# Optimization experiments

Measured on AMD Instinct MI355X. Metric: run time of the kernel, lower is better.

The kernel has to match this reference:

```python
import jax, jax.numpy as jnp
import numpy as np

N_NODES = 100000
N_EDGES = 3200000
N_FEAT = 300
HIDDEN = 32
N_CLASSES = 10


def setup_inputs() -> dict:
    key = jax.random.key(0)
    k1, k2, k3, k4 = jax.random.split(key, 4)
    x = jax.random.normal(k1, (N_NODES, N_FEAT), dtype=jnp.float32)
    edge_index = jax.random.randint(k2, (2, N_EDGES), 0, N_NODES, dtype=jnp.int64)
    # Glorot-ish init for weights
    W1 = jax.random.normal(k3, (N_FEAT, HIDDEN), dtype=jnp.float32) * (1.0 / np.sqrt(N_FEAT))
    b1 = jnp.zeros((HIDDEN,), dtype=jnp.float32)
    W2 = jax.random.normal(k4, (HIDDEN, N_CLASSES), dtype=jnp.float32) * (1.0 / np.sqrt(HIDDEN))
    b2 = jnp.zeros((N_CLASSES,), dtype=jnp.float32)
    return {"x": x, "edge_index": edge_index, "W1": W1, "b1": b1, "W2": W2, "b2": b2}


def reference(x, edge_index, W1, b1, W2, b2):
    N = x.shape[0]
    # GCNConv default: add self-loops, symmetric normalization deg^-1/2 A deg^-1/2
    loops = jnp.arange(N, dtype=edge_index.dtype)
    src = jnp.concatenate([edge_index[0], loops])  # message sources
    dst = jnp.concatenate([edge_index[1], loops])  # aggregation targets

    deg = jax.ops.segment_sum(jnp.ones(dst.shape, dtype=x.dtype), dst, num_segments=N)
    dinv = jnp.where(deg > 0, jax.lax.rsqrt(deg), 0.0)
    norm = dinv[src] * dinv[dst]  # [E+N]

    def gcn_conv(h, W, b):
        h = h @ W                                   # [N, out] dense GEMM first (linear-then-propagate)
        msg = h[src] * norm[:, None]                # gather + scale
        out = jax.ops.segment_sum(msg, dst, num_segments=N)  # scatter-add aggregate
        return out + b

    h = jnp.tanh(gcn_conv(x, W1, b1))
    # dropout p=0.5 is identity in eval mode (training=False)
    logits = gcn_conv(h, W2, b2)
    return jax.nn.log_softmax(logits, axis=1)
```

## Files before the change

kernel.cpp:

```cpp
#include <hip/hip_runtime.h>
#include <math.h>
#include <float.h>

#define NFEAT 300
#define HID 32
#define NCLS 10
#define GP 16
#define BSZ 128
#define TILE 8192
#define XS 264

typedef unsigned int uint;

__device__ __forceinline__ unsigned short f2bf(float f) {
    uint u = __float_as_uint(f);
    u += 0x7FFFu + ((u >> 16) & 1u);
    return (unsigned short)(u >> 16);
}
__device__ __forceinline__ uint pack2(float a, float b) {
    return (uint)f2bf(a) | ((uint)f2bf(b) << 16);
}
__device__ __forceinline__ float4 cvt4(uint2 v) {
    return make_float4(__uint_as_float(v.x << 16),
                       __uint_as_float(v.x & 0xFFFF0000u),
                       __uint_as_float(v.y << 16),
                       __uint_as_float(v.y & 0xFFFF0000u));
}

__global__ void k_zero_i(int* __restrict__ p, int n) {
    int i = blockIdx.x * 256 + threadIdx.x;
    if (i < n) p[i] = 0;
}

__global__ __launch_bounds__(256) void k_bhist(const int* __restrict__ ei, int E, int NB,
                                               int* __restrict__ bcnt) {
    __shared__ int h[1024];
    for (int i = threadIdx.x; i < NB; i += 256) h[i] = 0;
    __syncthreads();
    for (long long i = (long long)blockIdx.x * 256 + threadIdx.x; i < E;
         i += (long long)gridDim.x * 256)
        atomicAdd(&h[ei[E + i] >> 7], 1);
    __syncthreads();
    for (int i = threadIdx.x; i < NB; i += 256) {
        int v = h[i];
        if (v) atomicAdd(&bcnt[i], v);
    }
}

__global__ void k_bscan(const int* __restrict__ bcnt, int NB, int E,
                        int* __restrict__ bases, int* __restrict__ bcur) {
    __shared__ int s[1024];
    int tid = threadIdx.x;
    int v = (tid < NB) ? bcnt[tid] : 0;
    s[tid] = v;
    __syncthreads();
    for (int off = 1; off < 1024; off <<= 1) {
        int t = (tid >= off) ? s[tid - off] : 0;
        __syncthreads();
        s[tid] += t;
        __syncthreads();
    }
    if (tid < NB) {
        int ex = s[tid] - v;
        bases[tid] = ex;
        bcur[tid] = ex;
        if (tid == NB - 1) bases[NB] = E;
    }
}

__global__ __launch_bounds__(256) void k_part(const int* __restrict__ ei, int E, int NB,
                                              int* __restrict__ bcur, int* __restrict__ pp) {
    __shared__ int hist[1024], lbase[1024], gbase[1024], lcur[1024];
    __shared__ int stage[TILE], tgt[TILE];
    int* part = gbase;
    int tid = threadIdx.x;
    long long t0 = (long long)blockIdx.x * TILE;
    int nE = (int)(((long long)E - t0 < TILE) ? ((long long)E - t0) : TILE);

    for (int b = tid; b < NB; b += 256) hist[b] = 0;
    __syncthreads();
    for (int i = tid; i < nE; i += 256) {
        int d = ei[E + t0 + i];
        atomicAdd(&hist[d >> 7], 1);
    }
    __syncthreads();
    int i0 = tid * 4;
    int c0 = (i0 + 0 < NB) ? hist[i0 + 0] : 0;
    int c1 = (i0 + 1 < NB) ? hist[i0 + 1] : 0;
    int c2 = (i0 + 2 < NB) ? hist[i0 + 2] : 0;
    int c3 = (i0 + 3 < NB) ? hist[i0 + 3] : 0;
    int sum = c0 + c1 + c2 + c3;
    part[tid] = sum;
    __syncthreads();
    for (int off = 1; off < 256; off <<= 1) {
        int t = (tid >= off) ? part[tid - off] : 0;
        __syncthreads();
        part[tid] += t;
        __syncthreads();
    }
    int ex = part[tid] - sum;
    if (i0 + 0 < NB) { lbase[i0 + 0] = ex; ex += c0; }
    if (i0 + 1 < NB) { lbase[i0 + 1] = ex; ex += c1; }
    if (i0 + 2 < NB) { lbase[i0 + 2] = ex; ex += c2; }
    if (i0 + 3 < NB) { lbase[i0 + 3] = ex; ex += c3; }
    __syncthreads();
    for (int b = tid; b < NB; b += 256) {
        int h = hist[b];
        gbase[b] = h ? atomicAdd(&bcur[b], h) : 0;
        lcur[b] = 0;
    }
    __syncthreads();
    for (int i = tid; i < nE; i += 256) {
        int s = ei[t0 + i];
        int d = ei[E + t0 + i];
        int b = d >> 7;
        int lo = atomicAdd(&lcur[b], 1);
        int slot = lbase[b] + lo;
        stage[slot] = ((d - (b << 7)) << 17) | s;
        tgt[slot] = gbase[b] + lo;
    }
    __syncthreads();
    for (int i = tid; i < nE; i += 256)
        pp[tgt[i]] = stage[i];
}

__global__ __launch_bounds__(256) void k_csr(const int* __restrict__ pp,
                                             const int* __restrict__ bases,
                                             int N, int E,
                                             int* __restrict__ rowptr,
                                             float* __restrict__ dinv,
                                             int* __restrict__ col) {
    __shared__ int lc[BSZ], rp[BSZ], sc[BSZ];
    int b = blockIdx.x, tid = threadIdx.x;
    int n0 = b << 7;
    int base = bases[b];
    int cnt = bases[b + 1] - base;
    if (tid < BSZ) lc[tid] = 0;
    __syncthreads();
    for (int i = tid; i < cnt; i += 256)
        atomicAdd(&lc[pp[base + i] >> 17], 1);
    __syncthreads();
    if (tid < BSZ) sc[tid] = lc[tid];
    __syncthreads();
    for (int off = 1; off < BSZ; off <<= 1) {
        int t = (tid < BSZ && tid >= off) ? sc[tid - off] : 0;
        __syncthreads();
        if (tid < BSZ) sc[tid] += t;
        __syncthreads();
    }
    if (tid < BSZ) {
        int node = n0 + tid;
        int ex = base + sc[tid] - lc[tid];
        rp[tid] = ex;
        if (node < N) {
            rowptr[node] = ex;
            dinv[node] = rsqrtf((float)(lc[tid] + 1));
            if (node == N - 1) rowptr[N] = E;
        }
        lc[tid] = 0;
    }
    __syncthreads();
    for (int i = tid; i < cnt; i += 256) {
        int v = pp[base + i];
        int dl = v >> 17;
        int lo = atomicAdd(&lc[dl], 1);
        col[rp[dl] + lo] = v & 0x1FFFF;
    }
}

__global__ __launch_bounds__(256) void k_gemm1(const float* __restrict__ x,
                                               const float* __restrict__ W1,
                                               const float* __restrict__ dinv,
                                               uint* __restrict__ h1s, int n) {
    __shared__ float xs[2][24 * XS];
    __shared__ float Wc[2][24 * HID];
    const int tid = threadIdx.x;
    const int lane = tid & 63;
    const int w = __builtin_amdgcn_readfirstlane(tid >> 6);
    const int n0 = blockIdx.x * 256;
    const float4* x4 = reinterpret_cast<const float4*>(x);
    const float4* w4 = reinterpret_cast<const float4*>(W1);

    float acc[32];
#pragma unroll
    for (int i = 0; i < 32; ++i) acc[i] = 0.f;

    float4 u[6];
    float4 wreg;
#pragma unroll
    for (int m = 0; m < 6; ++m) {
        int idx = m * 256 + tid, r = idx / 6, fq = idx % 6;
        u[m] = x4[(size_t)min(n0 + r, n - 1) * 75 + fq];
    }
    if (tid < 192) wreg = w4[tid];

    int cur = 0;
    for (int ch = 0; ch < 13; ++ch) {
        const int CL = (ch == 12) ? 12 : 24;
        if (CL == 24) {
#pragma unroll
            for (int m = 0; m < 6; ++m) {
                int idx = m * 256 + tid, r = idx / 6, fq = idx % 6;
                float* d = &xs[cur][(fq * 4) * XS + r];
                d[0] = u[m].x; d[XS] = u[m].y; d[2 * XS] = u[m].z; d[3 * XS] = u[m].w;
            }
            if (tid < 192) reinterpret_cast<float4*>(Wc[cur])[tid] = wreg;
        } else {
#pragma unroll
            for (int m = 0; m < 3; ++m) {
                int idx = m * 256 + tid, r = idx / 3, fq = idx % 3;
                float* d = &xs[cur][(fq * 4) * XS + r];
                d[0] = u[m].x; d[XS] = u[m].y; d[2 * XS] = u[m].z; d[3 * XS] = u[m].w;
            }
            if (tid < 96) reinterpret_cast<float4*>(Wc[cur])[tid] = wreg;
        }
        __syncthreads();
        if (ch < 12) {
            int nch = ch + 1;
            if (nch < 12) {
#pragma unroll
                for (int m = 0; m < 6; ++m) {
                    int idx = m * 256 + tid, r = idx / 6, fq = idx % 6;
                    u[m] = x4[(size_t)min(n0 + r, n - 1) * 75 + nch * 6 + fq];
                }
                if (tid < 192) wreg = w4[nch * 192 + tid];
            } else {
#pragma unroll
                for (int m = 0; m < 3; ++m) {
                    int idx = m * 256 + tid, r = idx / 3, fq = idx % 3;
                    u[m] = x4[(size_t)min(n0 + r, n - 1) * 75 + 72 + fq];
                }
                if (tid < 96) wreg = w4[12 * 192 + tid];
            }
        }
        const float* xr = &xs[cur][4 * lane];
        const float* wr = &Wc[cur][8 * w];
#pragma unroll 4
        for (int j = 0; j < CL; ++j) {
            float4 xv = *reinterpret_cast<const float4*>(xr + j * XS);
            float4 w0 = *reinterpret_cast<const float4*>(wr + j * HID);
            float4 w1 = *reinterpret_cast<const float4*>(wr + j * HID + 4);
            float xn[4] = {xv.x, xv.y, xv.z, xv.w};
            float wk[8] = {w0.x, w0.y, w0.z, w0.w, w1.x, w1.y, w1.z, w1.w};
#pragma unroll
            for (int nn = 0; nn < 4; ++nn)
#pragma unroll
                for (int kk = 0; kk < 8; ++kk)
                    acc[nn * 8 + kk] = fmaf(xn[nn], wk[kk], acc[nn * 8 + kk]);
        }
        cur ^= 1;
    }
    float4 dv = reinterpret_cast<const float4*>(dinv + n0)[lane];
    float dvv[4] = {dv.x, dv.y, dv.z, dv.w};
#pragma unroll
    for (int nn = 0; nn < 4; ++nn) {
        int node = n0 + 4 * lane + nn;
        if (node < n) {
            float dd = dvv[nn];
            uint4 o;
            o.x = pack2(dd * acc[nn * 8 + 0], dd * acc[nn * 8 + 1]);
            o.y = pack2(dd * acc[nn * 8 + 2], dd * acc[nn * 8 + 3]);
            o.z = pack2(dd * acc[nn * 8 + 4], dd * acc[nn * 8 + 5]);
            o.w = pack2(dd * acc[nn * 8 + 6], dd * acc[nn * 8 + 7]);
            reinterpret_cast<uint4*>(h1s)[(size_t)node * 4 + w] = o;
        }
    }
}

__global__ __launch_bounds__(256) void k_agg1(const uint2* __restrict__ h1s,
                                              const int* __restrict__ rowptr,
                                              const int* __restrict__ col,
                                              const float* __restrict__ dinv,
                                              const float* __restrict__ b1,
                                              float* __restrict__ h2, int n) {
    int node = blockIdx.x * 32 + (threadIdx.x >> 3);
    int l = threadIdx.x & 7;
    if (node >= n) return;
    int beg = rowptr[node], end = rowptr[node + 1];
    float4 a0 = cvt4(h1s[(size_t)node * 8 + l]);
    float4 a1 = make_float4(0.f, 0.f, 0.f, 0.f);
    float4 a2 = make_float4(0.f, 0.f, 0.f, 0.f);
    float4 a3 = make_float4(0.f, 0.f, 0.f, 0.f);
    int j = beg;
    for (; j + 3 < end; j += 4) {
        int s0 = col[j], s1 = col[j + 1], s2 = col[j + 2], s3 = col[j + 3];
        uint2 u0 = h1s[(size_t)s0 * 8 + l];
        uint2 u1 = h1s[(size_t)s1 * 8 + l];
        uint2 u2 = h1s[(size_t)s2 * 8 + l];
        uint2 u3 = h1s[(size_t)s3 * 8 + l];
        float4 v0 = cvt4(u0), v1 = cvt4(u1), v2 = cvt4(u2), v3 = cvt4(u3);
        a0.x += v0.x; a0.y += v0.y; a0.z += v0.z; a0.w += v0.w;
        a1.x += v1.x; a1.y += v1.y; a1.z += v1.z; a1.w += v1.w;
        a2.x += v2.x; a2.y += v2.y; a2.z += v2.z; a2.w += v2.w;
        a3.x += v3.x; a3.y += v3.y; a3.z += v3.z; a3.w += v3.w;
    }
    for (; j < end; ++j) {
        float4 v = cvt4(h1s[(size_t)col[j] * 8 + l]);
        a0.x += v.x; a0.y += v.y; a0.z += v.z; a0.w += v.w;
    }
    float dd = dinv[node];
    const float4* b4 = reinterpret_cast<const float4*>(b1);
    float4 bv = b4[l];
    float4 r;
    r.x = tanhf(fmaf(dd, (a0.x + a1.x) + (a2.x + a3.x), bv.x));
    r.y = tanhf(fmaf(dd, (a0.y + a1.y) + (a2.y + a3.y), bv.y));
    r.z = tanhf(fmaf(dd, (a0.z + a1.z) + (a2.z + a3.z), bv.z));
    r.w = tanhf(fmaf(dd, (a0.w + a1.w) + (a2.w + a3.w), bv.w));
    reinterpret_cast<float4*>(h2)[(size_t)node * 8 + l] = r;
}

__global__ __launch_bounds__(256) void k_gemm2(const float* __restrict__ h2,
                                               const float* __restrict__ W2,
                                               const float* __restrict__ dinv,
                                               unsigned short* __restrict__ gs, int n) {
    __shared__ float Ws[HID * NCLS];
    for (int i = threadIdx.x; i < HID * NCLS; i += 256) Ws[i] = W2[i];
    __syncthreads();
    int t = blockIdx.x * 256 + threadIdx.x;
    int node = t >> 4, c = t & 15;
    if (node >= n || c >= NCLS) return;
    const float* hr = h2 + (size_t)node * HID;
    float acc = 0.f;
#pragma unroll
    for (int k = 0; k < HID; ++k) acc = fmaf(hr[k], Ws[k * NCLS + c], acc);
    gs[(size_t)node * GP + c] = f2bf(acc * dinv[node]);
}

__global__ __launch_bounds__(256) void k_agg2(const uint2* __restrict__ gs,
                                              const int* __restrict__ rowptr,
                                              const int* __restrict__ col,
                                              const float* __restrict__ dinv,
                                              const float* __restrict__ b2,
                                              float* __restrict__ out, int n) {
    int node = blockIdx.x * 64 + (threadIdx.x >> 2);
    int l = threadIdx.x & 3;
    if (node >= n) return;
    int beg = rowptr[node], end = rowptr[node + 1];
    float4 a0 = cvt4(gs[(size_t)node * 4 + l]);
    float4 a1 = make_float4(0.f, 0.f, 0.f, 0.f);
    int j = beg;
    for (; j + 1 < end; j += 2) {
        int s0 = col[j], s1 = col[j + 1];
        uint2 u0 = gs[(size_t)s0 * 4 + l];
        uint2 u1 = gs[(size_t)s1 * 4 + l];
        float4 v0 = cvt4(u0), v1 = cvt4(u1);
        a0.x += v0.x; a0.y += v0.y; a0.z += v0.z; a0.w += v0.w;
        a1.x += v1.x; a1.y += v1.y; a1.z += v1.z; a1.w += v1.w;
    }
    if (j < end) {
        float4 v = cvt4(gs[(size_t)col[j] * 4 + l]);
        a0.x += v.x; a0.y += v.y; a0.z += v.z; a0.w += v.w;
    }
    float dd = dinv[node];
    int c0 = 4 * l;
    float val[4];
    float av[4] = {a0.x + a1.x, a0.y + a1.y, a0.z + a1.z, a0.w + a1.w};
#pragma unroll
    for (int i = 0; i < 4; ++i) {
        int c = c0 + i;
        val[i] = (c < NCLS) ? fmaf(dd, av[i], b2[c]) : -FLT_MAX;
    }
    float m = fmaxf(fmaxf(val[0], val[1]), fmaxf(val[2], val[3]));
    m = fmaxf(m, __shfl_xor(m, 1, 4));
    m = fmaxf(m, __shfl_xor(m, 2, 4));
    float s = 0.f;
#pragma unroll
    for (int i = 0; i < 4; ++i)
        if (c0 + i < NCLS) s += expf(val[i] - m);
    s += __shfl_xor(s, 1, 4);
    s += __shfl_xor(s, 2, 4);
    float ls = m + logf(s);
    float* orow = out + (size_t)node * NCLS;
#pragma unroll
    for (int i = 0; i < 4; ++i)
        if (c0 + i < NCLS) orow[c0 + i] = val[i] - ls;
}

static inline size_t align256(size_t b) { return (b + 255) & ~(size_t)255; }

extern "C" void kernel_launch(void* const* d_in, const int* in_sizes, int n_in,
                              void* d_out, int out_size, void* d_ws, size_t ws_size,
                              hipStream_t stream) {
    const float* x  = (const float*)d_in[0];
    const int*   ei = (const int*)d_in[1];
    const float* W1 = (const float*)d_in[2];
    const float* b1 = (const float*)d_in[3];
    const float* W2 = (const float*)d_in[4];
    const float* b2 = (const float*)d_in[5];
    float* out = (float*)d_out;

    const int N = in_sizes[0] / NFEAT;
    const int E = in_sizes[1] / 2;
    const int NB = (N + BSZ - 1) / BSZ;

    char* p = (char*)d_ws;
    int* bcnt   = (int*)p;  p += align256(1024 * 4);
    int* bases  = (int*)p;  p += align256(1025 * 4);
    int* bcur   = (int*)p;  p += align256(1024 * 4);
    int* rowptr = (int*)p;  p += align256((size_t)(N + 1) * 4);
    int* pp     = (int*)p;  p += align256((size_t)E * 4);
    int* col    = (int*)p;  p += align256((size_t)E * 4);
    float* dinv = (float*)p; p += align256((size_t)N * 4);
    uint* h1s   = (uint*)p;  p += align256((size_t)N * HID * 2);
    float* h2   = (float*)p; p += align256((size_t)N * HID * 4);
    unsigned short* gsb = (unsigned short*)h1s;

    dim3 B(256);
    int nT = (E + TILE - 1) / TILE;

    k_zero_i<<<4, B, 0, stream>>>(bcnt, 1024);
    k_bhist<<<128, B, 0, stream>>>(ei, E, NB, bcnt);
    k_bscan<<<1, 1024, 0, stream>>>(bcnt, NB, E, bases, bcur);
    k_part<<<nT, B, 0, stream>>>(ei, E, NB, bcur, pp);
    k_csr<<<NB, B, 0, stream>>>(pp, bases, N, E, rowptr, dinv, col);

    k_gemm1<<<(N + 255) / 256, B, 0, stream>>>(x, W1, dinv, h1s, N);
    k_agg1<<<(N + 31) / 32, B, 0, stream>>>((const uint2*)h1s, rowptr, col, dinv, b1, h2, N);
    k_gemm2<<<(N * 16 + 255) / 256, B, 0, stream>>>(h2, W2, dinv, gsb, N);
    k_agg2<<<(N + 63) / 64, B, 0, stream>>>((const uint2*)gsb, rowptr, col, dinv, b2, out, N);
}
```

Measured before the change: 237.5 us.

## Use bf16 MFMA matrix cores for first-layer dense GEMM

Replaces the FP32 scalar-FMA register-tiled GEMM for x@W1 with bf16 MFMA 16x16x32 instructions. x is converted to bf16 as it is staged into a row-major LDS tile, and W1 is transposed and converted to bf16 once per block, with K zero-padded to 320. The aim is to cut ALU time in the GEMM, which reads 120MB of x and is likely memory-bound. The trade-off is reduced input precision (bf16 x and W) and a heavier per-block W1 preload.

```diff
diff --git a/kernel.cpp b/kernel.cpp
--- a/kernel.cpp
+++ b/kernel.cpp
@@ -8,7 +8,8 @@
 #define GP 16
 #define BSZ 128
 #define TILE 8192
-#define XS 264
+#define WT_S 328
+#define XR_S 40
 
 typedef unsigned int uint;
 
@@ -172,97 +173,113 @@
                                                const float* __restrict__ W1,
                                                const float* __restrict__ dinv,
                                                uint* __restrict__ h1s, int n) {
-    __shared__ float xs[2][24 * XS];
-    __shared__ float Wc[2][24 * HID];
+    typedef __attribute__((ext_vector_type(8))) short bf16x8;
+    typedef __attribute__((ext_vector_type(4))) float f32x4;
+    __shared__ unsigned short Wt[32 * WT_S];
+    __shared__ unsigned short xs[2][256 * XR_S];
     const int tid = threadIdx.x;
     const int lane = tid & 63;
-    const int w = __builtin_amdgcn_readfirstlane(tid >> 6);
+    const int w = tid >> 6;
     const int n0 = blockIdx.x * 256;
     const float4* x4 = reinterpret_cast<const float4*>(x);
-    const float4* w4 = reinterpret_cast<const float4*>(W1);
-
-    float acc[32];
-#pragma unroll
-    for (int i = 0; i < 32; ++i) acc[i] = 0.f;
-
-    float4 u[6];
-    float4 wreg;
-#pragma unroll
-    for (int m = 0; m < 6; ++m) {
-        int idx = m * 256 + tid, r = idx / 6, fq = idx % 6;
-        u[m] = x4[(size_t)min(n0 + r, n - 1) * 75 + fq];
-    }
-    if (tid < 192) wreg = w4[tid];
-
+    unsigned short* h1u = reinterpret_cast<unsigned short*>(h1s);
+
+    float4 u[8];
+#pragma unroll
+    for (int m = 0; m < 8; ++m) {
+        int idx = m * 256 + tid, node = idx >> 3, f = idx & 7;
+        u[m] = x4[(size_t)min(n0 + node, n - 1) * 75 + f];
+    }
+    {
+        const float4* w4 = reinterpret_cast<const float4*>(W1);
+        for (int idx = tid; idx < 2400; idx += 256) {
+            float4 v = w4[idx];
+            int j = idx >> 3, o = (idx & 7) * 4;
+            Wt[(o + 0) * WT_S + j] = f2bf(v.x);
+            Wt[(o + 1) * WT_S + j] = f2bf(v.y);
+            Wt[(o + 2) * WT_S + j] = f2bf(v.z);
+            Wt[(o + 3) * WT_S + j] = f2bf(v.w);
+        }
+        for (int i = tid; i < 32 * 20; i += 256) {
+            int o = i / 20, j = 300 + i % 20;
+            Wt[o * WT_S + j] = 0;
+        }
+    }
+
+    f32x4 acc[4][2];
+#pragma unroll
+    for (int t = 0; t < 4; ++t)
+#pragma unroll
+        for (int h = 0; h < 2; ++h) acc[t][h] = (f32x4){0.f, 0.f, 0.f, 0.f};
+
+    const int kb = (lane >> 4) << 3;
+    const int cl = lane & 15;
     int cur = 0;
-    for (int ch = 0; ch < 13; ++ch) {
-        const int CL = (ch == 12) ? 12 : 24;
-        if (CL == 24) {
-#pragma unroll
-            for (int m = 0; m < 6; ++m) {
-                int idx = m * 256 + tid, r = idx / 6, fq = idx % 6;
-                float* d = &xs[cur][(fq * 4) * XS + r];
-                d[0] = u[m].x; d[XS] = u[m].y; d[2 * XS] = u[m].z; d[3 * XS] = u[m].w;
-            }
-            if (tid < 192) reinterpret_cast<float4*>(Wc[cur])[tid] = wreg;
+    for (int ch = 0; ch < 10; ++ch) {
+        if (ch < 9) {
+#pragma unroll
+            for (int m = 0; m < 8; ++m) {
+                int idx = m * 256 + tid, node = idx >> 3, f = idx & 7;
+                uint2 pk;
+                pk.x = pack2(u[m].x, u[m].y);
+                pk.y = pack2(u[m].z, u[m].w);
+                *reinterpret_cast<uint2*>(&xs[cur][node * XR_S + f * 4]) = pk;
+            }
         } else {
 #pragma unroll
             for (int m = 0; m < 3; ++m) {
-                int idx = m * 256 + tid, r = idx / 3, fq = idx % 3;
-                float* d = &xs[cur][(fq * 4) * XS + r];
-                d[0] = u[m].x; d[XS] = u[m].y; d[2 * XS] = u[m].z; d[3 * XS] = u[m].w;
-            }
-            if (tid < 96) reinterpret_cast<float4*>(Wc[cur])[tid] = wreg;
-        }
-        __syncthreads();
-        if (ch < 12) {
-            int nch = ch + 1;
-            if (nch < 12) {
-#pragma unroll
-                for (int m = 0; m < 6; ++m) {
-                    int idx = m * 256 + tid, r = idx / 6, fq = idx % 6;
-                    u[m] = x4[(size_t)min(n0 + r, n - 1) * 75 + nch * 6 + fq];
-                }
-                if (tid < 192) wreg = w4[nch * 192 + tid];
-            } else {
-#pragma unroll
-                for (int m = 0; m < 3; ++m) {
-                    int idx = m * 256 + tid, r = idx / 3, fq = idx % 3;
-                    u[m] = x4[(size_t)min(n0 + r, n - 1) * 75 + 72 + fq];
-                }
-                if (tid < 96) wreg = w4[12 * 192 + tid];
-            }
-        }
-        const float* xr = &xs[cur][4 * lane];
-        const float* wr = &Wc[cur][8 * w];
-#pragma unroll 4
-        for (int j = 0; j < CL; ++j) {
-            float4 xv = *reinterpret_cast<const float4*>(xr + j * XS);
-            float4 w0 = *reinterpret_cast<const float4*>(wr + j * HID);
-            float4 w1 = *reinterpret_cast<const float4*>(wr + j * HID + 4);
-            float xn[4] = {xv.x, xv.y, xv.z, xv.w};
-            float wk[8] = {w0.x, w0.y, w0.z, w0.w, w1.x, w1.y, w1.z, w1.w};
-#pragma unroll
-            for (int nn = 0; nn < 4; ++nn)
-#pragma unroll
-                for (int kk = 0; kk < 8; ++kk)
-                    acc[nn * 8 + kk] = fmaf(xn[nn], wk[kk], acc[nn * 8 + kk]);
+                int idx = m * 256 + tid, node = idx / 3, f = idx % 3;
+                uint2 pk;
+                pk.x = pack2(u[m].x, u[m].y);
+                pk.y = pack2(u[m].z, u[m].w);
+                *reinterpret_cast<uint2*>(&xs[cur][node * XR_S + f * 4]) = pk;
+            }
+            uint2 z; z.x = 0u; z.y = 0u;
+#pragma unroll
+            for (int m = 0; m < 5; ++m) {
+                int idx = m * 256 + tid, node = idx / 5, slot = 3 + idx % 5;
+                *reinterpret_cast<uint2*>(&xs[cur][node * XR_S + slot * 4]) = z;
+            }
+        }
+        __syncthreads();
+        if (ch + 1 < 9) {
+#pragma unroll
+            for (int m = 0; m < 8; ++m) {
+                int idx = m * 256 + tid, node = idx >> 3, f = idx & 7;
+                u[m] = x4[(size_t)min(n0 + node, n - 1) * 75 + (ch + 1) * 8 + f];
+            }
+        } else if (ch + 1 == 9) {
+#pragma unroll
+            for (int m = 0; m < 3; ++m) {
+                int idx = m * 256 + tid, node = idx / 3, f = idx % 3;
+                u[m] = x4[(size_t)min(n0 + node, n - 1) * 75 + 72 + f];
+            }
+        }
+        const unsigned short* xb = xs[cur];
+        bf16x8 b0 = *reinterpret_cast<const bf16x8*>(&Wt[cl * WT_S + ch * 32 + kb]);
+        bf16x8 b1 = *reinterpret_cast<const bf16x8*>(&Wt[(cl + 16) * WT_S + ch * 32 + kb]);
+#pragma unroll
+        for (int t = 0; t < 4; ++t) {
+            bf16x8 a = *reinterpret_cast<const bf16x8*>(
+                &xb[(w * 64 + t * 16 + cl) * XR_S + kb]);
+            acc[t][0] = __builtin_amdgcn_mfma_f32_16x16x32_bf16(a, b0, acc[t][0], 0, 0, 0);
+            acc[t][1] = __builtin_amdgcn_mfma_f32_16x16x32_bf16(a, b1, acc[t][1], 0, 0, 0);
         }
         cur ^= 1;
     }
-    float4 dv = reinterpret_cast<const float4*>(dinv + n0)[lane];
-    float dvv[4] = {dv.x, dv.y, dv.z, dv.w};
-#pragma unroll
-    for (int nn = 0; nn < 4; ++nn) {
-        int node = n0 + 4 * lane + nn;
-        if (node < n) {
-            float dd = dvv[nn];
-            uint4 o;
-            o.x = pack2(dd * acc[nn * 8 + 0], dd * acc[nn * 8 + 1]);
-            o.y = pack2(dd * acc[nn * 8 + 2], dd * acc[nn * 8 + 3]);
-            o.z = pack2(dd * acc[nn * 8 + 4], dd * acc[nn * 8 + 5]);
-            o.w = pack2(dd * acc[nn * 8 + 6], dd * acc[nn * 8 + 7]);
-            reinterpret_cast<uint4*>(h1s)[(size_t)node * 4 + w] = o;
+    const int rq = (lane >> 4) * 4;
+#pragma unroll
+    for (int t = 0; t < 4; ++t) {
+        int nb = n0 + w * 64 + t * 16 + rq;
+        float4 dv = *reinterpret_cast<const float4*>(&dinv[nb]);
+        float dr[4] = {dv.x, dv.y, dv.z, dv.w};
+#pragma unroll
+        for (int r = 0; r < 4; ++r) {
+            int node = nb + r;
+            if (node < n) {
+                h1u[(size_t)node * 32 + cl]      = f2bf(dr[r] * acc[t][0][r]);
+                h1u[(size_t)node * 32 + 16 + cl] = f2bf(dr[r] * acc[t][1][r]);
+            }
         }
     }
 }
```

After: 212.0 us. 10.7% less time.
